# Optimization experiments

Measured on AMD Instinct MI355X. Metric: run time of the kernel, lower is better.

Reference implementation:

```python
import jax, jax.numpy as jnp
import numpy as np

NUM_CLASSES = 21
THRESH = 0.5
NEGPOS = 3
VAR0, VAR1 = 0.1, 0.2
FEAT = 19
N_ANCH = 9
B = 256
NUM_OBJS = 12
P = FEAT * FEAT * N_ANCH  # 3249


def make_priors():
    # 19x19 grid, 3 scales x 3 aspect ratios (1, 2, 1/2) -> 9 anchors/cell, center form
    cxy = (np.arange(FEAT, dtype=np.float32) + 0.5) / FEAT
    cx, cy = np.meshgrid(cxy, cxy, indexing='ij')  # [19,19]
    scales = np.array([0.1, 0.2, 0.35], dtype=np.float32)
    ratios = np.array([1.0, 2.0, 0.5], dtype=np.float32)
    w = (scales[:, None] * np.sqrt(ratios)[None, :]).reshape(-1)  # [9]
    h = (scales[:, None] / np.sqrt(ratios)[None, :]).reshape(-1)
    cx = np.broadcast_to(cx[:, :, None], (FEAT, FEAT, N_ANCH))
    cy = np.broadcast_to(cy[:, :, None], (FEAT, FEAT, N_ANCH))
    w = np.broadcast_to(w[None, None, :], (FEAT, FEAT, N_ANCH))
    h = np.broadcast_to(h[None, None, :], (FEAT, FEAT, N_ANCH))
    pri = np.stack([cx, cy, w, h], axis=-1).reshape(-1, 4)
    return jnp.asarray(np.clip(pri, 1e-3, 1.0))


def setup_inputs() -> dict:
    key = jax.random.key(0)
    k1, k2, k3, k4, k5 = jax.random.split(key, 5)
    loc_data = jax.random.normal(k1, (B, P, 4), dtype=jnp.float32)
    conf_data = jax.random.normal(k2, (B, P, NUM_CLASSES), dtype=jnp.float32)
    priors = make_priors()
    xy = jax.random.uniform(k3, (B, NUM_OBJS, 2), minval=0.05, maxval=0.65)
    wh = jax.random.uniform(k4, (B, NUM_OBJS, 2), minval=0.05, maxval=0.30)
    labels = jax.random.randint(k5, (B, NUM_OBJS), 0, NUM_CLASSES - 1).astype(jnp.float32)
    targets = jnp.concatenate([xy, xy + wh, labels[..., None]], axis=-1)  # [B,O,5]
    return {"loc_data": loc_data, "conf_data": conf_data, "priors": priors, "targets": targets}


def point_form(boxes):  # (cx,cy,w,h) -> (x1,y1,x2,y2)
    return jnp.concatenate([boxes[:, :2] - boxes[:, 2:] / 2,
                            boxes[:, :2] + boxes[:, 2:] / 2], axis=1)


def jaccard(a, b):  # a: [n,4], b: [m,4] point form -> [n,m]
    lt = jnp.maximum(a[:, None, :2], b[None, :, :2])
    rb = jnp.minimum(a[:, None, 2:], b[None, :, 2:])
    inter = jnp.prod(jnp.clip(rb - lt, 0.0, None), axis=-1)
    area_a = jnp.prod(a[:, 2:] - a[:, :2], axis=-1)
    area_b = jnp.prod(b[:, 2:] - b[:, :2], axis=-1)
    return inter / (area_a[:, None] + area_b[None, :] - inter)


def encode(matched, priors):  # matched point-form [P,4], priors center-form [P,4]
    g_cxcy = ((matched[:, :2] + matched[:, 2:]) / 2 - priors[:, :2]) / (VAR0 * priors[:, 2:])
    g_wh = jnp.log((matched[:, 2:] - matched[:, :2]) / priors[:, 2:]) / VAR1
    return jnp.concatenate([g_cxcy, g_wh], axis=1)


def match_one(truths, labels, priors, priors_pt):
    overlaps = jaccard(truths, priors_pt)          # [O,P]
    best_prior_idx = jnp.argmax(overlaps, axis=1)  # [O]
    best_truth_ov = jnp.max(overlaps, axis=0)      # [P]
    best_truth_idx = jnp.argmax(overlaps, axis=0)  # [P]
    best_truth_ov = best_truth_ov.at[best_prior_idx].set(2.0)
    best_truth_idx = best_truth_idx.at[best_prior_idx].set(jnp.arange(truths.shape[0]))
    matches = truths[best_truth_idx]               # [P,4]
    conf = labels[best_truth_idx] + 1
    conf = jnp.where(best_truth_ov < THRESH, 0, conf)
    return encode(matches, priors), conf


def reference(loc_data, conf_data, priors, targets):
    truths = targets[:, :, :4]
    labels = targets[:, :, 4].astype(jnp.int32)
    priors_pt = point_form(priors)
    loc_t, conf_t = jax.vmap(lambda t, l: match_one(t, l, priors, priors_pt))(truths, labels)
    loc_t = jax.lax.stop_gradient(loc_t)
    conf_t = jax.lax.stop_gradient(conf_t)

    pos = conf_t > 0                                               # [B,P]
    # smooth L1 (sum) over matched priors
    d = loc_data - loc_t
    ad = jnp.abs(d)
    sl1 = jnp.where(ad < 1.0, 0.5 * d * d, ad - 0.5)
    loss_l = jnp.sum(sl1 * pos[..., None].astype(sl1.dtype))

    # per-prior CE = logsumexp - logit[target]
    lse = jax.nn.logsumexp(conf_data, axis=-1)                     # [B,P]
    gathered = jnp.take_along_axis(conf_data, conf_t[..., None], axis=2)[..., 0]
    ce = lse - gathered                                            # [B,P]

    # hard negative mining: double argsort rank of neg losses
    loss_c_mine = jnp.where(pos, 0.0, ce)
    loss_idx = jnp.argsort(-loss_c_mine, axis=1)
    idx_rank = jnp.argsort(loss_idx, axis=1)
    num_pos = jnp.sum(pos, axis=1, keepdims=True)                  # [B,1]
    num_neg = jnp.minimum(NEGPOS * num_pos, P - 1)
    neg = idx_rank < num_neg

    sel = pos | neg
    loss_c = jnp.sum(jnp.where(sel, ce, 0.0))

    have_centerloss = jnp.max(sel.reshape(B, FEAT, FEAT, N_ANCH), axis=3).reshape(-1)
    conf_t_featuremap = jnp.max(conf_t.reshape(B, FEAT, FEAT, N_ANCH), axis=3).reshape(-1)

    N = jnp.sum(num_pos).astype(loc_data.dtype)
    return loss_l / N, loss_c / N, conf_t_featuremap, have_centerloss
```

## Files before the change

### kernel.cpp

```cpp
#include <hip/hip_runtime.h>
#include <math.h>

#pragma clang fp contract(off)

#define BB      256
#define PP      3249
#define NCLS    21
#define NOBJ    12
#define CELLS   361
#define THRESH_ 0.5f


__global__ __launch_bounds__(1024) void fused_kernel(
    const float* __restrict__ loc, const float* __restrict__ conf,
    const float* __restrict__ priors, const float* __restrict__ targets,
    int* __restrict__ numpos, double* __restrict__ lossl,
    double* __restrict__ lossc, float* __restrict__ out)
{
    const int b = blockIdx.x, tid = threadIdx.x;
    const int lane = tid & 63, wid = tid >> 6;

    __shared__ float s_tx1[NOBJ], s_ty1[NOBJ], s_tx2[NOBJ], s_ty2[NOBJ];
    __shared__ float s_area_t[NOBJ];
    __shared__ int   s_label[NOBJ];
    __shared__ float s_bov[PP];
    __shared__ short s_bidx[PP];
    __shared__ int   s_bpi[NOBJ];
    __shared__ float s_wov[NOBJ][16];
    __shared__ int   s_widx[NOBJ][16];
    __shared__ unsigned long long s_key[PP];
    __shared__ unsigned char s_ct[PP];
    __shared__ unsigned char s_sel[PP];
    __shared__ int s_hist[256];
    __shared__ int s_chosen, s_knext, s_nneg;
    __shared__ double s_pl[16];
    __shared__ int    s_pn[16];
    __shared__ double s_pc[16];

    if (tid < NOBJ) {
        const float* t = targets + ((size_t)b * NOBJ + tid) * 5;
        float x1 = t[0], y1 = t[1], x2 = t[2], y2 = t[3];
        s_tx1[tid] = x1; s_ty1[tid] = y1; s_tx2[tid] = x2; s_ty2[tid] = y2;
        s_label[tid] = (int)t[4];
        s_area_t[tid] = (x2 - x1) * (y2 - y1);
    }
    __syncthreads();

    float l_bov[NOBJ];
    int   l_bidx[NOBJ];
#pragma unroll
    for (int j = 0; j < NOBJ; ++j) { l_bov[j] = -1.0f; l_bidx[j] = 0x7FFFFFFF; }

    for (int p = tid; p < PP; p += 1024) {
        float cx = priors[4*p+0], cy = priors[4*p+1], w = priors[4*p+2], h = priors[4*p+3];
        float px1 = cx - w / 2.0f, py1 = cy - h / 2.0f;
        float px2 = cx + w / 2.0f, py2 = cy + h / 2.0f;
        float area_p = (px2 - px1) * (py2 - py1);
        float bov = -1.0f; int bidx = 0;
#pragma unroll
        for (int j = 0; j < NOBJ; ++j) {
            float ltx = fmaxf(s_tx1[j], px1);
            float lty = fmaxf(s_ty1[j], py1);
            float rbx = fminf(s_tx2[j], px2);
            float rby = fminf(s_ty2[j], py2);
            float iw = fmaxf(rbx - ltx, 0.0f);
            float ih = fmaxf(rby - lty, 0.0f);
            float inter = iw * ih;
            float iou = inter / ((s_area_t[j] + area_p) - inter);
            if (iou > bov) { bov = iou; bidx = j; }
            if (iou > l_bov[j]) { l_bov[j] = iou; l_bidx[j] = p; }
        }
        s_bov[p] = bov;
        s_bidx[p] = (short)bidx;
    }

#pragma unroll
    for (int j = 0; j < NOBJ; ++j) {
        float ov = l_bov[j]; int ix = l_bidx[j];
#pragma unroll
        for (int off = 32; off > 0; off >>= 1) {
            float ov2 = __shfl_xor(ov, off);
            int   ix2 = __shfl_xor(ix, off);
            if (ov2 > ov || (ov2 == ov && ix2 < ix)) { ov = ov2; ix = ix2; }
        }
        if (lane == 0) { s_wov[j][wid] = ov; s_widx[j][wid] = ix; }
    }
    __syncthreads();
    if (tid < NOBJ) {
        float ov = s_wov[tid][0]; int ix = s_widx[tid][0];
#pragma unroll
        for (int w2 = 1; w2 < 16; ++w2) {
            float ov2 = s_wov[tid][w2]; int ix2 = s_widx[tid][w2];
            if (ov2 > ov || (ov2 == ov && ix2 < ix)) { ov = ov2; ix = ix2; }
        }
        s_bpi[tid] = ix;
    }
    __syncthreads();

    int my_pos = 0;
    double my_lossl = 0.0;
    const float* confb = conf + (size_t)b * PP * NCLS;
    for (int p = tid; p < PP; p += 1024) {
        int jov = -1;
#pragma unroll
        for (int j = 0; j < NOBJ; ++j) if (s_bpi[j] == p) jov = j;
        int idx; float ov;
        if (jov >= 0) { idx = jov; ov = 2.0f; }
        else          { idx = (int)s_bidx[p]; ov = s_bov[p]; }
        int c = (ov < THRESH_) ? 0 : (s_label[idx] + 1);
        s_ct[p] = (unsigned char)c;

        const float* cd = confb + (size_t)p * NCLS;
        float m = cd[0];
#pragma unroll
        for (int k = 1; k < NCLS; ++k) m = fmaxf(m, cd[k]);
        float s = 0.0f;
#pragma unroll
        for (int k = 0; k < NCLS; ++k) s += expf(cd[k] - m);
        float ce = (logf(s) + m) - cd[c];

        float v = (c > 0) ? 0.0f : ce;
        s_key[p] = ((unsigned long long)__float_as_uint(v) << 32)
                 | (unsigned int)(0xFFFFFFFFu - (unsigned int)p);
        s_bov[p] = ce;

        if (c > 0) {
            ++my_pos;
            float cx = priors[4*p+0], cy = priors[4*p+1], w = priors[4*p+2], h = priors[4*p+3];
            float m0 = s_tx1[idx], m1 = s_ty1[idx], m2 = s_tx2[idx], m3 = s_ty2[idx];
            float g0 = ((m0 + m2) / 2.0f - cx) / (0.1f * w);
            float g1 = ((m1 + m3) / 2.0f - cy) / (0.1f * h);
            float g2 = logf((m2 - m0) / w) / 0.2f;
            float g3 = logf((m3 - m1) / h) / 0.2f;
            const float* ld = loc + ((size_t)b * PP + p) * 4;
            float d0 = ld[0] - g0, d1 = ld[1] - g1, d2 = ld[2] - g2, d3 = ld[3] - g3;
            float a0 = fabsf(d0), a1 = fabsf(d1), a2 = fabsf(d2), a3 = fabsf(d3);
            my_lossl += (double)((a0 < 1.0f) ? 0.5f * d0 * d0 : a0 - 0.5f);
            my_lossl += (double)((a1 < 1.0f) ? 0.5f * d1 * d1 : a1 - 0.5f);
            my_lossl += (double)((a2 < 1.0f) ? 0.5f * d2 * d2 : a2 - 0.5f);
            my_lossl += (double)((a3 < 1.0f) ? 0.5f * d3 * d3 : a3 - 0.5f);
        }
    }
#pragma unroll
    for (int off = 32; off > 0; off >>= 1) {
        my_lossl += __shfl_down(my_lossl, off);
        my_pos   += __shfl_down(my_pos, off);
    }
    if (lane == 0) { s_pl[wid] = my_lossl; s_pn[wid] = my_pos; }
    __syncthreads();
    if (tid == 0) {
        double L = 0.0; int n = 0;
#pragma unroll
        for (int w2 = 0; w2 < 16; ++w2) { L += s_pl[w2]; n += s_pn[w2]; }
        lossl[b] = L; numpos[b] = n;
        s_nneg = min(3 * n, PP - 1);
    }
    __syncthreads();

    unsigned long long prefix = 0ull, pmask = 0ull;
    int kk = s_nneg;
    for (int d = 56; d >= 0; d -= 8) {
        if (tid < 256) s_hist[tid] = 0;
        __syncthreads();
        for (int i = tid; i < PP; i += 1024) {
            unsigned long long key = s_key[i];
            if ((key & pmask) == prefix)
                atomicAdd(&s_hist[(int)((key >> d) & 0xFF)], 1);
        }
        __syncthreads();
        if (tid < 64) {
            int h0 = s_hist[4*lane+0], h1 = s_hist[4*lane+1];
            int h2 = s_hist[4*lane+2], h3 = s_hist[4*lane+3];
            int ls = h0 + h1 + h2 + h3;
            int x = ls;
#pragma unroll
            for (int off = 1; off < 64; off <<= 1) {
                int y = __shfl_down(x, off);
                if (lane + off < 64) x += y;
            }
            int excl = x - ls;
            int cb3 = excl;
            int cb2 = cb3 + h3;
            int cb1 = cb2 + h2;
            int cb0 = cb1 + h1;
            if (cb3 < kk && kk <= cb3 + h3) { s_chosen = 4*lane+3; s_knext = kk - cb3; }
            if (cb2 < kk && kk <= cb2 + h2) { s_chosen = 4*lane+2; s_knext = kk - cb2; }
            if (cb1 < kk && kk <= cb1 + h1) { s_chosen = 4*lane+1; s_knext = kk - cb1; }
            if (cb0 < kk && kk <= cb0 + h0) { s_chosen = 4*lane+0; s_knext = kk - cb0; }
        }
        __syncthreads();
        prefix |= ((unsigned long long)(unsigned int)s_chosen) << d;
        pmask  |= 0xFFull << d;
        kk = s_knext;
        __syncthreads();
    }
    const unsigned long long kth = prefix;

    double my_c = 0.0;
    for (int p = tid; p < PP; p += 1024) {
        int c = s_ct[p];
        bool sel = (c > 0) || (s_key[p] >= kth);
        s_sel[p] = sel ? 1 : 0;
        if (sel) my_c += (double)s_bov[p];
    }
    __syncthreads();

    for (int cI = tid; cI < CELLS; cI += 1024) {
        int mc = 0, hv = 0;
#pragma unroll
        for (int a = 0; a < 9; ++a) {
            int p = cI * 9 + a;
            int cv = s_ct[p];
            mc = (cv > mc) ? cv : mc;
            hv |= s_sel[p];
        }
        out[2 + (size_t)b * CELLS + cI] = (float)mc;
        out[2 + (size_t)BB * CELLS + (size_t)b * CELLS + cI] = (float)hv;
    }

#pragma unroll
    for (int off = 32; off > 0; off >>= 1) my_c += __shfl_down(my_c, off);
    if (lane == 0) s_pc[wid] = my_c;
    __syncthreads();
    if (tid == 0) {
        double L = 0.0;
#pragma unroll
        for (int w2 = 0; w2 < 16; ++w2) L += s_pc[w2];
        lossc[b] = L;
    }
}

__global__ __launch_bounds__(256) void finalize_kernel(
    const int* __restrict__ numpos, const double* __restrict__ lossl,
    const double* __restrict__ lossc, float* __restrict__ out)
{
    __shared__ double s_l[256], s_c[256];
    __shared__ int s_n[256];
    int tid = threadIdx.x;
    s_n[tid] = numpos[tid];
    s_l[tid] = lossl[tid];
    s_c[tid] = lossc[tid];
    __syncthreads();
    for (int s = 128; s > 0; s >>= 1) {
        if (tid < s) { s_n[tid] += s_n[tid + s]; s_l[tid] += s_l[tid + s]; s_c[tid] += s_c[tid + s]; }
        __syncthreads();
    }
    if (tid == 0) {
        double N = (double)s_n[0];
        out[0] = (float)(s_l[0] / N);
        out[1] = (float)(s_c[0] / N);
    }
}

extern "C" void kernel_launch(void* const* d_in, const int* in_sizes, int n_in,
                              void* d_out, int out_size, void* d_ws, size_t ws_size,
                              hipStream_t stream) {
    const float* loc     = (const float*)d_in[0];
    const float* conf    = (const float*)d_in[1];
    const float* priors  = (const float*)d_in[2];
    const float* targets = (const float*)d_in[3];
    float* out = (float*)d_out;

    double* ws_lossl  = (double*)d_ws;
    double* ws_lossc  = ws_lossl + BB;
    int*    ws_numpos = (int*)(ws_lossc + BB);

    hipLaunchKernelGGL(fused_kernel, dim3(BB), dim3(1024), 0, stream,
                       loc, conf, priors, targets, ws_numpos, ws_lossl, ws_lossc, out);
    hipLaunchKernelGGL(finalize_kernel, dim3(1), dim3(256), 0, stream,
                       ws_numpos, ws_lossl, ws_lossc, out);
}
```

Measured before the change: 141.1 us.

## Split fused kernel into wide IoU/logsumexp pass and per-batch selection pass

The IoU matching and the per-prior logsumexp over the conf tensor move into a first kernel launched on a 13x256 grid of 256-thread blocks. That kernel writes lse, best overlap and best index to workspace, and reduces the best prior per object with 64-bit atomicMax. The original design had only 256 blocks, each streaming 3249x21 floats, which limited memory parallelism. The second kernel keeps the per-batch hard-negative radix selection but reads the precomputed values. The cost is extra global traffic for the intermediates, a memset, an extra launch, and a re-read of conf for the gathered logit.

```diff
diff --git a/kernel.cpp b/kernel.cpp
--- a/kernel.cpp
+++ b/kernel.cpp
@@ -9,54 +9,37 @@
 #define NOBJ    12
 #define CELLS   361
 #define THRESH_ 0.5f
-
-
-__global__ __launch_bounds__(1024) void fused_kernel(
-    const float* __restrict__ loc, const float* __restrict__ conf,
-    const float* __restrict__ priors, const float* __restrict__ targets,
-    int* __restrict__ numpos, double* __restrict__ lossl,
-    double* __restrict__ lossc, float* __restrict__ out)
+#define NPB     13
+
+
+__global__ __launch_bounds__(256) void k1_lse_iou(
+    const float* __restrict__ conf, const float* __restrict__ priors,
+    const float* __restrict__ targets,
+    float* __restrict__ g_lse, float* __restrict__ g_bov,
+    unsigned char* __restrict__ g_bidx, unsigned long long* __restrict__ g_best)
 {
-    const int b = blockIdx.x, tid = threadIdx.x;
-    const int lane = tid & 63, wid = tid >> 6;
+    const int b = blockIdx.y;
+    const int tid = threadIdx.x, lane = tid & 63;
+    const int p = blockIdx.x * 256 + tid;
+    const bool valid = (p < PP);
 
     __shared__ float s_tx1[NOBJ], s_ty1[NOBJ], s_tx2[NOBJ], s_ty2[NOBJ];
     __shared__ float s_area_t[NOBJ];
-    __shared__ int   s_label[NOBJ];
-    __shared__ float s_bov[PP];
-    __shared__ short s_bidx[PP];
-    __shared__ int   s_bpi[NOBJ];
-    __shared__ float s_wov[NOBJ][16];
-    __shared__ int   s_widx[NOBJ][16];
-    __shared__ unsigned long long s_key[PP];
-    __shared__ unsigned char s_ct[PP];
-    __shared__ unsigned char s_sel[PP];
-    __shared__ int s_hist[256];
-    __shared__ int s_chosen, s_knext, s_nneg;
-    __shared__ double s_pl[16];
-    __shared__ int    s_pn[16];
-    __shared__ double s_pc[16];
-
     if (tid < NOBJ) {
         const float* t = targets + ((size_t)b * NOBJ + tid) * 5;
         float x1 = t[0], y1 = t[1], x2 = t[2], y2 = t[3];
         s_tx1[tid] = x1; s_ty1[tid] = y1; s_tx2[tid] = x2; s_ty2[tid] = y2;
-        s_label[tid] = (int)t[4];
         s_area_t[tid] = (x2 - x1) * (y2 - y1);
     }
     __syncthreads();
 
-    float l_bov[NOBJ];
-    int   l_bidx[NOBJ];
-#pragma unroll
-    for (int j = 0; j < NOBJ; ++j) { l_bov[j] = -1.0f; l_bidx[j] = 0x7FFFFFFF; }
-
-    for (int p = tid; p < PP; p += 1024) {
+    float iou_j[NOBJ];
+    float bov = -1.0f; int bidx = 0;
+    if (valid) {
         float cx = priors[4*p+0], cy = priors[4*p+1], w = priors[4*p+2], h = priors[4*p+3];
         float px1 = cx - w / 2.0f, py1 = cy - h / 2.0f;
         float px2 = cx + w / 2.0f, py2 = cy + h / 2.0f;
         float area_p = (px2 - px1) * (py2 - py1);
-        float bov = -1.0f; int bidx = 0;
 #pragma unroll
         for (int j = 0; j < NOBJ; ++j) {
             float ltx = fmaxf(s_tx1[j], px1);
@@ -67,33 +50,76 @@
             float ih = fmaxf(rby - lty, 0.0f);
             float inter = iw * ih;
             float iou = inter / ((s_area_t[j] + area_p) - inter);
+            iou_j[j] = iou;
             if (iou > bov) { bov = iou; bidx = j; }
-            if (iou > l_bov[j]) { l_bov[j] = iou; l_bidx[j] = p; }
-        }
-        s_bov[p] = bov;
-        s_bidx[p] = (short)bidx;
+        }
+    } else {
+#pragma unroll
+        for (int j = 0; j < NOBJ; ++j) iou_j[j] = -1.0f;
     }
 
 #pragma unroll
     for (int j = 0; j < NOBJ; ++j) {
-        float ov = l_bov[j]; int ix = l_bidx[j];
+        float ov = iou_j[j]; int ix = valid ? p : 0x7FFFFFFF;
 #pragma unroll
         for (int off = 32; off > 0; off >>= 1) {
             float ov2 = __shfl_xor(ov, off);
             int   ix2 = __shfl_xor(ix, off);
             if (ov2 > ov || (ov2 == ov && ix2 < ix)) { ov = ov2; ix = ix2; }
         }
-        if (lane == 0) { s_wov[j][wid] = ov; s_widx[j][wid] = ix; }
-    }
-    __syncthreads();
+        if (lane == 0 && ov >= 0.0f) {
+            unsigned long long key =
+                ((unsigned long long)__float_as_uint(ov) << 32)
+                | (unsigned int)(0xFFFFFFFFu - (unsigned int)ix);
+            atomicMax(&g_best[b * NOBJ + j], key);
+        }
+    }
+
+    if (valid) {
+        const size_t bp = (size_t)b * PP + p;
+        g_bov[bp] = bov;
+        g_bidx[bp] = (unsigned char)bidx;
+
+        const float* cd = conf + bp * NCLS;
+        float m = cd[0];
+#pragma unroll
+        for (int k = 1; k < NCLS; ++k) m = fmaxf(m, cd[k]);
+        float s = 0.0f;
+#pragma unroll
+        for (int k = 0; k < NCLS; ++k) s += expf(cd[k] - m);
+        g_lse[bp] = logf(s) + m;
+    }
+}
+
+__global__ __launch_bounds__(1024) void k2_select(
+    const float* __restrict__ loc, const float* __restrict__ conf,
+    const float* __restrict__ priors, const float* __restrict__ targets,
+    const float* __restrict__ g_lse, const float* __restrict__ g_bov,
+    const unsigned char* __restrict__ g_bidx, const unsigned long long* __restrict__ g_best,
+    int* __restrict__ numpos, double* __restrict__ lossl,
+    double* __restrict__ lossc, float* __restrict__ out)
+{
+    const int b = blockIdx.x, tid = threadIdx.x;
+    const int lane = tid & 63, wid = tid >> 6;
+
+    __shared__ float s_tx1[NOBJ], s_ty1[NOBJ], s_tx2[NOBJ], s_ty2[NOBJ];
+    __shared__ int   s_label[NOBJ];
+    __shared__ int   s_bpi[NOBJ];
+    __shared__ unsigned long long s_key[PP];
+    __shared__ float s_ce[PP];
+    __shared__ unsigned char s_ct[PP];
+    __shared__ unsigned char s_sel[PP];
+    __shared__ int s_hist[256];
+    __shared__ int s_chosen, s_knext, s_nneg;
+    __shared__ double s_pl[16];
+    __shared__ int    s_pn[16];
+    __shared__ double s_pc[16];
+
     if (tid < NOBJ) {
-        float ov = s_wov[tid][0]; int ix = s_widx[tid][0];
-#pragma unroll
-        for (int w2 = 1; w2 < 16; ++w2) {
-            float ov2 = s_wov[tid][w2]; int ix2 = s_widx[tid][w2];
-            if (ov2 > ov || (ov2 == ov && ix2 < ix)) { ov = ov2; ix = ix2; }
-        }
-        s_bpi[tid] = ix;
+        const float* t = targets + ((size_t)b * NOBJ + tid) * 5;
+        s_tx1[tid] = t[0]; s_ty1[tid] = t[1]; s_tx2[tid] = t[2]; s_ty2[tid] = t[3];
+        s_label[tid] = (int)t[4];
+        s_bpi[tid] = (int)(0xFFFFFFFFu - (unsigned int)(g_best[b * NOBJ + tid] & 0xFFFFFFFFull));
     }
     __syncthreads();
 
@@ -101,28 +127,21 @@
     double my_lossl = 0.0;
     const float* confb = conf + (size_t)b * PP * NCLS;
     for (int p = tid; p < PP; p += 1024) {
+        const size_t bp = (size_t)b * PP + p;
         int jov = -1;
 #pragma unroll
         for (int j = 0; j < NOBJ; ++j) if (s_bpi[j] == p) jov = j;
         int idx; float ov;
         if (jov >= 0) { idx = jov; ov = 2.0f; }
-        else          { idx = (int)s_bidx[p]; ov = s_bov[p]; }
+        else          { idx = (int)g_bidx[bp]; ov = g_bov[bp]; }
         int c = (ov < THRESH_) ? 0 : (s_label[idx] + 1);
         s_ct[p] = (unsigned char)c;
 
-        const float* cd = confb + (size_t)p * NCLS;
-        float m = cd[0];
-#pragma unroll
-        for (int k = 1; k < NCLS; ++k) m = fmaxf(m, cd[k]);
-        float s = 0.0f;
-#pragma unroll
-        for (int k = 0; k < NCLS; ++k) s += expf(cd[k] - m);
-        float ce = (logf(s) + m) - cd[c];
-
+        float ce = g_lse[bp] - confb[(size_t)p * NCLS + c];
+        s_ce[p] = ce;
         float v = (c > 0) ? 0.0f : ce;
         s_key[p] = ((unsigned long long)__float_as_uint(v) << 32)
                  | (unsigned int)(0xFFFFFFFFu - (unsigned int)p);
-        s_bov[p] = ce;
 
         if (c > 0) {
             ++my_pos;
@@ -132,7 +151,7 @@
             float g1 = ((m1 + m3) / 2.0f - cy) / (0.1f * h);
             float g2 = logf((m2 - m0) / w) / 0.2f;
             float g3 = logf((m3 - m1) / h) / 0.2f;
-            const float* ld = loc + ((size_t)b * PP + p) * 4;
+            const float* ld = loc + (bp) * 4;
             float d0 = ld[0] - g0, d1 = ld[1] - g1, d2 = ld[2] - g2, d3 = ld[3] - g3;
             float a0 = fabsf(d0), a1 = fabsf(d1), a2 = fabsf(d2), a3 = fabsf(d3);
             my_lossl += (double)((a0 < 1.0f) ? 0.5f * d0 * d0 : a0 - 0.5f);
@@ -201,7 +220,7 @@
         int c = s_ct[p];
         bool sel = (c > 0) || (s_key[p] >= kth);
         s_sel[p] = sel ? 1 : 0;
-        if (sel) my_c += (double)s_bov[p];
+        if (sel) my_c += (double)s_ce[p];
     }
     __syncthreads();
 
@@ -263,10 +282,19 @@
 
     double* ws_lossl  = (double*)d_ws;
     double* ws_lossc  = ws_lossl + BB;
-    int*    ws_numpos = (int*)(ws_lossc + BB);
-
-    hipLaunchKernelGGL(fused_kernel, dim3(BB), dim3(1024), 0, stream,
-                       loc, conf, priors, targets, ws_numpos, ws_lossl, ws_lossc, out);
+    unsigned long long* ws_best = (unsigned long long*)(ws_lossc + BB);
+    int*    ws_numpos = (int*)(ws_best + (size_t)BB * NOBJ);
+    float*  ws_lse    = (float*)(ws_numpos + BB);
+    float*  ws_bov    = ws_lse + (size_t)BB * PP;
+    unsigned char* ws_bidx = (unsigned char*)(ws_bov + (size_t)BB * PP);
+
+    hipMemsetAsync(ws_best, 0, (size_t)BB * NOBJ * sizeof(unsigned long long), stream);
+
+    hipLaunchKernelGGL(k1_lse_iou, dim3(NPB, BB), dim3(256), 0, stream,
+                       conf, priors, targets, ws_lse, ws_bov, ws_bidx, ws_best);
+    hipLaunchKernelGGL(k2_select, dim3(BB), dim3(1024), 0, stream,
+                       loc, conf, priors, targets, ws_lse, ws_bov, ws_bidx, ws_best,
+                       ws_numpos, ws_lossl, ws_lossc, out);
     hipLaunchKernelGGL(finalize_kernel, dim3(1), dim3(256), 0, stream,
                        ws_numpos, ws_lossl, ws_lossc, out);
 }
```

New measurement: 157.3 us. 11.4% more time.

## Stage conf rows through LDS tiles and shorten radix select passes

Applied to the files above, without the earlier changes.

The per-prior conf reads are restaged so each batch row's conf data is copied into shared memory in 256-row tiles with coalesced float4/float2 loads chosen by alignment, and then each thread reads its 21 logits from LDS. Per-prior match info is packed into a byte, which frees the float/short shared arrays, and positive CE is accumulated during the tile pass while negative CE is taken back out of the sort key. The radix select skips two of its byte passes because the low index bits above 16 are always 0xFFFF, given P < 65536. The cost is 13 barrier-separated tile phases in which only 256 of 1024 threads do the compute, which reduces parallelism in that stage.

```diff
diff --git a/kernel.cpp b/kernel.cpp
--- a/kernel.cpp
+++ b/kernel.cpp
@@ -9,6 +9,8 @@
 #define NOBJ    12
 #define CELLS   361
 #define THRESH_ 0.5f
+#define TROWS   256
+#define NTILE   13
 
 
 __global__ __launch_bounds__(1024) void fused_kernel(
@@ -20,22 +22,19 @@
     const int b = blockIdx.x, tid = threadIdx.x;
     const int lane = tid & 63, wid = tid >> 6;
 
-    __shared__ float s_tx1[NOBJ], s_ty1[NOBJ], s_tx2[NOBJ], s_ty2[NOBJ];
-    __shared__ float s_area_t[NOBJ];
-    __shared__ int   s_label[NOBJ];
-    __shared__ float s_bov[PP];
-    __shared__ short s_bidx[PP];
-    __shared__ int   s_bpi[NOBJ];
-    __shared__ float s_wov[NOBJ][16];
-    __shared__ int   s_widx[NOBJ][16];
+    __shared__ float s_conf[TROWS * NCLS];
     __shared__ unsigned long long s_key[PP];
+    __shared__ unsigned char s_mi[PP];
     __shared__ unsigned char s_ct[PP];
     __shared__ unsigned char s_sel[PP];
     __shared__ int s_hist[256];
+    __shared__ float s_tx1[NOBJ], s_ty1[NOBJ], s_tx2[NOBJ], s_ty2[NOBJ], s_area_t[NOBJ];
+    __shared__ int   s_label[NOBJ], s_bpi[NOBJ];
+    __shared__ float s_wov[NOBJ][16];
+    __shared__ int   s_widx[NOBJ][16];
+    __shared__ double s_pl[16], s_pc[16];
+    __shared__ int    s_pn[16];
     __shared__ int s_chosen, s_knext, s_nneg;
-    __shared__ double s_pl[16];
-    __shared__ int    s_pn[16];
-    __shared__ double s_pc[16];
 
     if (tid < NOBJ) {
         const float* t = targets + ((size_t)b * NOBJ + tid) * 5;
@@ -70,8 +69,7 @@
             if (iou > bov) { bov = iou; bidx = j; }
             if (iou > l_bov[j]) { l_bov[j] = iou; l_bidx[j] = p; }
         }
-        s_bov[p] = bov;
-        s_bidx[p] = (short)bidx;
+        s_mi[p] = (unsigned char)(((bov < THRESH_) ? 0 : 0x80) | bidx);
     }
 
 #pragma unroll
@@ -99,54 +97,83 @@
 
     int my_pos = 0;
     double my_lossl = 0.0;
+    double my_cpos = 0.0;
     const float* confb = conf + (size_t)b * PP * NCLS;
-    for (int p = tid; p < PP; p += 1024) {
-        int jov = -1;
-#pragma unroll
-        for (int j = 0; j < NOBJ; ++j) if (s_bpi[j] == p) jov = j;
-        int idx; float ov;
-        if (jov >= 0) { idx = jov; ov = 2.0f; }
-        else          { idx = (int)s_bidx[p]; ov = s_bov[p]; }
-        int c = (ov < THRESH_) ? 0 : (s_label[idx] + 1);
-        s_ct[p] = (unsigned char)c;
-
-        const float* cd = confb + (size_t)p * NCLS;
-        float m = cd[0];
-#pragma unroll
-        for (int k = 1; k < NCLS; ++k) m = fmaxf(m, cd[k]);
-        float s = 0.0f;
-#pragma unroll
-        for (int k = 0; k < NCLS; ++k) s += expf(cd[k] - m);
-        float ce = (logf(s) + m) - cd[c];
-
-        float v = (c > 0) ? 0.0f : ce;
-        s_key[p] = ((unsigned long long)__float_as_uint(v) << 32)
-                 | (unsigned int)(0xFFFFFFFFu - (unsigned int)p);
-        s_bov[p] = ce;
-
-        if (c > 0) {
-            ++my_pos;
-            float cx = priors[4*p+0], cy = priors[4*p+1], w = priors[4*p+2], h = priors[4*p+3];
-            float m0 = s_tx1[idx], m1 = s_ty1[idx], m2 = s_tx2[idx], m3 = s_ty2[idx];
-            float g0 = ((m0 + m2) / 2.0f - cx) / (0.1f * w);
-            float g1 = ((m1 + m3) / 2.0f - cy) / (0.1f * h);
-            float g2 = logf((m2 - m0) / w) / 0.2f;
-            float g3 = logf((m3 - m1) / h) / 0.2f;
-            const float* ld = loc + ((size_t)b * PP + p) * 4;
-            float d0 = ld[0] - g0, d1 = ld[1] - g1, d2 = ld[2] - g2, d3 = ld[3] - g3;
-            float a0 = fabsf(d0), a1 = fabsf(d1), a2 = fabsf(d2), a3 = fabsf(d3);
-            my_lossl += (double)((a0 < 1.0f) ? 0.5f * d0 * d0 : a0 - 0.5f);
-            my_lossl += (double)((a1 < 1.0f) ? 0.5f * d1 * d1 : a1 - 0.5f);
-            my_lossl += (double)((a2 < 1.0f) ? 0.5f * d2 * d2 : a2 - 0.5f);
-            my_lossl += (double)((a3 < 1.0f) ? 0.5f * d3 * d3 : a3 - 0.5f);
-        }
-    }
+    const int align4 = (b & 3);
+    for (int t = 0; t < NTILE; ++t) {
+        const int base = t * TROWS;
+        const int rows = (PP - base < TROWS) ? (PP - base) : TROWS;
+        const int nd = rows * NCLS;
+        const float* src = confb + (size_t)base * NCLS;
+        if (align4 == 0) {
+            const int nv = nd >> 2;
+            const float4* s4 = (const float4*)src;
+            float4* d4 = (float4*)s_conf;
+            for (int i = tid; i < nv; i += 1024) d4[i] = s4[i];
+            for (int i = (nv << 2) + tid; i < nd; i += 1024) s_conf[i] = src[i];
+        } else if ((align4 & 1) == 0) {
+            const int nv = nd >> 1;
+            const float2* s2 = (const float2*)src;
+            float2* d2 = (float2*)s_conf;
+            for (int i = tid; i < nv; i += 1024) d2[i] = s2[i];
+            for (int i = (nv << 1) + tid; i < nd; i += 1024) s_conf[i] = src[i];
+        } else {
+            for (int i = tid; i < nd; i += 1024) s_conf[i] = src[i];
+        }
+        __syncthreads();
+
+        if (tid < rows) {
+            const int p = base + tid;
+            int jov = -1;
+#pragma unroll
+            for (int j = 0; j < NOBJ; ++j) if (s_bpi[j] == p) jov = j;
+            const unsigned char mi = s_mi[p];
+            int idx, c;
+            if (jov >= 0) { idx = jov; c = s_label[idx] + 1; }
+            else { idx = mi & 15; c = (mi & 0x80) ? (s_label[idx] + 1) : 0; }
+            s_ct[p] = (unsigned char)c;
+
+            const float* cd = s_conf + tid * NCLS;
+            float m = cd[0];
+#pragma unroll
+            for (int k = 1; k < NCLS; ++k) m = fmaxf(m, cd[k]);
+            float s = 0.0f;
+#pragma unroll
+            for (int k = 0; k < NCLS; ++k) s += expf(cd[k] - m);
+            float ce = (logf(s) + m) - cd[c];
+
+            float v = (c > 0) ? 0.0f : ce;
+            s_key[p] = ((unsigned long long)__float_as_uint(v) << 32)
+                     | (unsigned int)(0xFFFFFFFFu - (unsigned int)p);
+
+            if (c > 0) {
+                ++my_pos;
+                my_cpos += (double)ce;
+                float cx = priors[4*p+0], cy = priors[4*p+1], w = priors[4*p+2], h = priors[4*p+3];
+                float m0 = s_tx1[idx], m1 = s_ty1[idx], m2 = s_tx2[idx], m3 = s_ty2[idx];
+                float g0 = ((m0 + m2) / 2.0f - cx) / (0.1f * w);
+                float g1 = ((m1 + m3) / 2.0f - cy) / (0.1f * h);
+                float g2 = logf((m2 - m0) / w) / 0.2f;
+                float g3 = logf((m3 - m1) / h) / 0.2f;
+                const float* ld = loc + ((size_t)b * PP + p) * 4;
+                float d0 = ld[0] - g0, d1 = ld[1] - g1, d2 = ld[2] - g2, d3 = ld[3] - g3;
+                float a0 = fabsf(d0), a1 = fabsf(d1), a2 = fabsf(d2), a3 = fabsf(d3);
+                my_lossl += (double)((a0 < 1.0f) ? 0.5f * d0 * d0 : a0 - 0.5f);
+                my_lossl += (double)((a1 < 1.0f) ? 0.5f * d1 * d1 : a1 - 0.5f);
+                my_lossl += (double)((a2 < 1.0f) ? 0.5f * d2 * d2 : a2 - 0.5f);
+                my_lossl += (double)((a3 < 1.0f) ? 0.5f * d3 * d3 : a3 - 0.5f);
+            }
+        }
+        __syncthreads();
+    }
+
+    double rl = my_lossl; int rp = my_pos;
 #pragma unroll
     for (int off = 32; off > 0; off >>= 1) {
-        my_lossl += __shfl_down(my_lossl, off);
-        my_pos   += __shfl_down(my_pos, off);
-    }
-    if (lane == 0) { s_pl[wid] = my_lossl; s_pn[wid] = my_pos; }
+        rl += __shfl_down(rl, off);
+        rp += __shfl_down(rp, off);
+    }
+    if (lane == 0) { s_pl[wid] = rl; s_pn[wid] = rp; }
     __syncthreads();
     if (tid == 0) {
         double L = 0.0; int n = 0;
@@ -157,9 +184,12 @@
     }
     __syncthreads();
 
+    const int ds[6] = {56, 48, 40, 32, 8, 0};
     unsigned long long prefix = 0ull, pmask = 0ull;
     int kk = s_nneg;
-    for (int d = 56; d >= 0; d -= 8) {
+#pragma unroll
+    for (int ri = 0; ri < 6; ++ri) {
+        const int d = ds[ri];
         if (tid < 256) s_hist[tid] = 0;
         __syncthreads();
         for (int i = tid; i < PP; i += 1024) {
@@ -192,16 +222,19 @@
         prefix |= ((unsigned long long)(unsigned int)s_chosen) << d;
         pmask  |= 0xFFull << d;
         kk = s_knext;
+        if (d == 32) { prefix |= 0xFFFF0000ull; pmask |= 0xFFFF0000ull; }
         __syncthreads();
     }
     const unsigned long long kth = prefix;
 
-    double my_c = 0.0;
+    double my_c = my_cpos;
     for (int p = tid; p < PP; p += 1024) {
         int c = s_ct[p];
-        bool sel = (c > 0) || (s_key[p] >= kth);
+        unsigned long long key = s_key[p];
+        bool sel = (c > 0) || (key >= kth);
         s_sel[p] = sel ? 1 : 0;
-        if (sel) my_c += (double)s_bov[p];
+        if (sel && c == 0)
+            my_c += (double)__uint_as_float((unsigned int)(key >> 32));
     }
     __syncthreads();
 
```

Result: slower. 179.9 us (+27.4%).
